# Kernel optimization log

Hardware: AMD Instinct MI355X
Metric: run time of the kernel (lower is better)

Reference implementation:

```python
import jax, jax.numpy as jnp
import numpy as np

EPS = 1e-8


def setup_inputs() -> dict:
    key = jax.random.key(0)
    ks = jax.random.split(key, 4)
    B, Cin, Cout, K, S, H, W = 16, 256, 256, 3, 512, 128, 128
    return {
        "x": jax.random.normal(ks[0], (B, Cin, H, W), dtype=jnp.float32),
        "style": jax.random.normal(ks[1], (B, S), dtype=jnp.float32),
        "weight": jax.random.normal(ks[2], (1, Cout, Cin, K, K), dtype=jnp.float32),
        "mod_w": jax.random.normal(ks[3], (Cin, S), dtype=jnp.float32) * (1.0 / np.sqrt(S)),
        "mod_b": jnp.zeros((Cin,), dtype=jnp.float32),
        "bias": jnp.zeros((1, Cout, 1, 1), dtype=jnp.float32),
    }


def reference(x, style, weight, mod_w, mod_b, bias):
    B, Cin, H, W = x.shape
    _, Cout, _, K, _ = weight.shape
    scale = 1.0 / np.sqrt(Cin * K * K)

    # modulation: Linear(style_dim -> in_channel)
    s = style @ mod_w.T + mod_b                      # [B, Cin]
    w = scale * weight * s[:, None, :, None, None]   # [B, Cout, Cin, K, K]
    demod = jax.lax.rsqrt(jnp.sum(w * w, axis=(2, 3, 4)) + EPS)  # [B, Cout]
    w = w * demod[:, :, None, None, None]

    # grouped conv with groups = batch (per-sample weights)
    w = w.reshape(B * Cout, Cin, K, K)
    xg = x.reshape(1, B * Cin, H, W)
    out = jax.lax.conv_general_dilated(
        xg, w,
        window_strides=(1, 1),
        padding=[(1, 1), (1, 1)],
        dimension_numbers=("NCHW", "OIHW", "NCHW"),
        feature_group_count=B,
    )
    Ho, Wo = out.shape[2], out.shape[3]
    out = out.reshape(B, Cout, Ho, Wo)
    return out + bias
```

## Files before the change

### kernel.cpp

```cpp
#include <hip/hip_runtime.h>
#include <stdint.h>

typedef unsigned short u16;
typedef __attribute__((ext_vector_type(8))) short short8;
typedef __attribute__((ext_vector_type(4))) float f32x4;

#define AS1 __attribute__((address_space(1)))
#define AS3 __attribute__((address_space(3)))

static __device__ __forceinline__ void gload_lds16(const void* g, void* l) {
  __builtin_amdgcn_global_load_lds((const AS1 void*)g, (AS3 void*)l, 16, 0, 0);
}

static __device__ __forceinline__ u16 bf16r(float f) {
  union { float f; uint32_t u; } c; c.f = f;
  uint32_t u = c.u;
  u += 0x7fffu + ((u >> 16) & 1u);
  return (u16)(u >> 16);
}

static constexpr int NB = 16, CIN = 256, COUT = 256, HW = 128, SDIM = 512;
static constexpr float SCALE = 1.0f / 48.0f;

__global__ void k_style(const float* __restrict__ style, const float* __restrict__ mod_w,
                        const float* __restrict__ mod_b, float* __restrict__ s) {
  int b = blockIdx.x, ci = threadIdx.x;
  const float4* st = (const float4*)(style + (size_t)b * SDIM);
  const float4* mw = (const float4*)(mod_w + (size_t)ci * SDIM);
  float acc = 0.f;
  #pragma unroll 4
  for (int j = 0; j < SDIM / 4; ++j) {
    float4 a = st[j], w = mw[j];
    acc += a.x * w.x + a.y * w.y + a.z * w.z + a.w * w.w;
  }
  s[b * CIN + ci] = acc + mod_b[ci];
}

__global__ void k_wmod(const float* __restrict__ weight, const float* __restrict__ s,
                       u16* __restrict__ Wb) {
  __shared__ float wld[CIN * 9];
  __shared__ float red[8];
  int bid = blockIdx.x;
  int b = bid >> 8, co = bid & 255;
  int t = threadIdx.x;
  const float* wsrc = weight + (size_t)co * (CIN * 9);
  for (int i = t; i < CIN * 9; i += 256) wld[i] = wsrc[i];
  __syncthreads();
  int ci = t;
  float sv = s[b * CIN + ci];
  float v[9];
  float sq = 0.f;
  #pragma unroll
  for (int k = 0; k < 9; ++k) {
    float w = SCALE * wld[ci * 9 + k] * sv;
    v[k] = w;
    sq += w * w;
  }
  #pragma unroll
  for (int off = 32; off; off >>= 1) sq += __shfl_down(sq, off);
  int lane = t & 63, wid = t >> 6;
  if (lane == 0) red[wid] = sq;
  __syncthreads();
  if (t == 0) red[4] = rsqrtf(red[0] + red[1] + red[2] + red[3] + 1e-8f);
  __syncthreads();
  float demod = red[4];
  #pragma unroll
  for (int k = 0; k < 9; ++k) {
    Wb[(((size_t)b * 9 + k) * COUT + co) * CIN + ci] = bf16r(v[k] * demod);
  }
}

__global__ void k_xt(const float* __restrict__ x, u16* __restrict__ xTp) {
  __shared__ u16 T[128 * 65];
  int bid = blockIdx.x;
  int b = bid >> 7, h = bid & 127;
  int t = threadIdx.x;
  size_t rowbase = (size_t)bid * 130 * CIN;
  xTp[rowbase + t] = 0;
  xTp[rowbase + (size_t)129 * CIN + t] = 0;
  for (int ci0 = 0; ci0 < CIN; ci0 += 64) {
    __syncthreads();
    #pragma unroll
    for (int i = 0; i < 8; ++i) {
      int idx = t + i * 256;
      int ci = idx >> 5, px4 = idx & 31;
      float4 v = *(const float4*)(x + (((size_t)b * CIN + ci0 + ci) * HW + h) * HW + px4 * 4);
      T[(px4 * 4 + 0) * 65 + ci] = bf16r(v.x);
      T[(px4 * 4 + 1) * 65 + ci] = bf16r(v.y);
      T[(px4 * 4 + 2) * 65 + ci] = bf16r(v.z);
      T[(px4 * 4 + 3) * 65 + ci] = bf16r(v.w);
    }
    __syncthreads();
    int ci = t & 63, pxo = t >> 6;
    #pragma unroll
    for (int i = 0; i < 32; ++i) {
      int px = i * 4 + pxo;
      xTp[rowbase + (size_t)(px + 1) * CIN + ci0 + ci] = T[px * 65 + ci];
    }
  }
}

__global__ __launch_bounds__(256, 2) void k_conv(const u16* __restrict__ Wb,
                                                 const u16* __restrict__ xTp,
                                                 const float* __restrict__ bias,
                                                 float* __restrict__ out) {
  __shared__ __align__(16) u16 As[128 * 64];
  __shared__ __align__(16) u16 Bs[128 * 64];
  int gid = blockIdx.x;
  int b = gid >> 8, r = gid & 255, cot = r >> 7, h = r & 127;
  int t = threadIdx.x, lane = t & 63, wid = t >> 6;
  int wr = wid >> 1, wc = wid & 1;

  f32x4 acc[4][4];
  #pragma unroll
  for (int i = 0; i < 4; ++i)
    #pragma unroll
    for (int j = 0; j < 4; ++j) acc[i][j] = (f32x4)0.f;

  int srow = wid * 8 + (lane >> 3);
  int scol = (lane & 7) * 8;

  for (int kh = 0; kh < 3; ++kh) {
    int hh = h + kh - 1;
    if ((unsigned)hh >= 128u) continue;
    for (int kw = 0; kw < 3; ++kw) {
      const u16* Ag0 = Wb + (((size_t)b * 9 + kh * 3 + kw) * COUT + cot * 128) * CIN;
      const u16* Bg0 = xTp + ((size_t)(b * 128 + hh) * 130 + kw) * CIN;
      for (int ci0 = 0; ci0 < CIN; ci0 += 64) {
        #pragma unroll
        for (int it = 0; it < 4; ++it) {
          int row = it * 32 + srow;
          gload_lds16(Ag0 + (size_t)row * CIN + ci0 + scol, &As[(it * 32 + wid * 8) * 64]);
        }
        #pragma unroll
        for (int it = 0; it < 4; ++it) {
          int row = it * 32 + srow;
          gload_lds16(Bg0 + (size_t)row * CIN + ci0 + scol, &Bs[(it * 32 + wid * 8) * 64]);
        }
        __syncthreads();
        #pragma unroll
        for (int kk = 0; kk < 2; ++kk) {
          short8 a[4], bb[4];
          #pragma unroll
          for (int mt = 0; mt < 4; ++mt)
            a[mt] = *(const short8*)&As[(wr * 64 + mt * 16 + (lane & 15)) * 64 + kk * 32 + (lane >> 4) * 8];
          #pragma unroll
          for (int nt = 0; nt < 4; ++nt)
            bb[nt] = *(const short8*)&Bs[(wc * 64 + nt * 16 + (lane & 15)) * 64 + kk * 32 + (lane >> 4) * 8];
          #pragma unroll
          for (int mt = 0; mt < 4; ++mt)
            #pragma unroll
            for (int nt = 0; nt < 4; ++nt)
              acc[mt][nt] = __builtin_amdgcn_mfma_f32_16x16x32_bf16(a[mt], bb[nt], acc[mt][nt], 0, 0, 0);
        }
        __syncthreads();
      }
    }
  }

  int colbase = wc * 64 + (lane & 15);
  int rowbase0 = cot * 128 + wr * 64 + ((lane >> 4) * 4);
  #pragma unroll
  for (int mt = 0; mt < 4; ++mt) {
    #pragma unroll
    for (int j = 0; j < 4; ++j) {
      int co = rowbase0 + mt * 16 + j;
      float bv = bias[co];
      float* orow = out + (((size_t)b * COUT + co) * HW + h) * HW;
      #pragma unroll
      for (int nt = 0; nt < 4; ++nt)
        orow[colbase + nt * 16] = acc[mt][nt][j] + bv;
    }
  }
}

extern "C" void kernel_launch(void* const* d_in, const int* in_sizes, int n_in,
                              void* d_out, int out_size, void* d_ws, size_t ws_size,
                              hipStream_t stream) {
  const float* x      = (const float*)d_in[0];
  const float* style  = (const float*)d_in[1];
  const float* weight = (const float*)d_in[2];
  const float* mod_w  = (const float*)d_in[3];
  const float* mod_b  = (const float*)d_in[4];
  const float* bias   = (const float*)d_in[5];
  float* out = (float*)d_out;

  char* ws = (char*)d_ws;
  float* s   = (float*)ws;
  u16* Wb    = (u16*)(ws + 16384);
  u16* xTp   = (u16*)(ws + 16384 + (size_t)NB * 9 * COUT * CIN * 2);

  k_style<<<NB, 256, 0, stream>>>(style, mod_w, mod_b, s);
  k_wmod<<<NB * COUT, 256, 0, stream>>>(weight, s, Wb);
  k_xt<<<NB * HW, 256, 0, stream>>>(x, xTp);
  k_conv<<<NB * 2 * HW, 256, 0, stream>>>(Wb, xTp, bias, out);
}
```

Measured before the change: 469.0 us.

## Restructure conv GEMM into 512-thread 256x128 tile with triple-buffered LDS pipeline

The conv kernel now uses 512-thread blocks that cover all 256 output channels for one image row, so each input tile is loaded once instead of twice. Global-to-LDS copies are triple-buffered with prefetch two k-steps ahead and explicit vmcnt waits, and MFMA phases run at raised wave priority. LDS columns are XOR-swizzled to avoid bank conflicts, and block IDs are remapped for locality. In exchange it needs 144KB of dynamic LDS at one block per CU, and it relies on hand-placed barriers and waitcnt values being correct.

```diff
diff --git a/kernel.cpp b/kernel.cpp
--- a/kernel.cpp
+++ b/kernel.cpp
@@ -100,16 +100,30 @@
   }
 }
 
-__global__ __launch_bounds__(256, 2) void k_conv(const u16* __restrict__ Wb,
+static constexpr int SLOTU = 24576;
+
+__global__ __launch_bounds__(512, 1) void k_conv(const u16* __restrict__ Wb,
                                                  const u16* __restrict__ xTp,
                                                  const float* __restrict__ bias,
                                                  float* __restrict__ out) {
-  __shared__ __align__(16) u16 As[128 * 64];
-  __shared__ __align__(16) u16 Bs[128 * 64];
-  int gid = blockIdx.x;
-  int b = gid >> 8, r = gid & 255, cot = r >> 7, h = r & 127;
+  extern __shared__ u16 lds[];
+  int bid = blockIdx.x;
+  int swz = (bid & 7) * 256 + (bid >> 3);
+  int b = swz >> 7, h = swz & 127;
+
   int t = threadIdx.x, lane = t & 63, wid = t >> 6;
   int wr = wid >> 1, wc = wid & 1;
+  int rowoff = wid * 8 + (lane >> 3);
+  int swzc = ((lane & 7) ^ (lane >> 3)) << 3;
+  int arow64 = (wr * 64 + (lane & 15)) * 64;
+  int brow64 = (wc * 64 + (lane & 15)) * 64;
+  int klo = (lane >> 4) * 8;
+  int cxor = (lane & 7) << 3;
+
+  const size_t wbB = (size_t)b * 9 * 256 * 256;
+
+  int ktbase = (h == 0) ? 12 : 0;
+  int nkt = 36 - ((h == 0) ? 12 : 0) - ((h == 127) ? 12 : 0);
 
   f32x4 acc[4][4];
   #pragma unroll
@@ -117,59 +131,114 @@
     #pragma unroll
     for (int j = 0; j < 4; ++j) acc[i][j] = (f32x4)0.f;
 
-  int srow = wid * 8 + (lane >> 3);
-  int scol = (lane & 7) * 8;
-
-  for (int kh = 0; kh < 3; ++kh) {
-    int hh = h + kh - 1;
-    if ((unsigned)hh >= 128u) continue;
-    for (int kw = 0; kw < 3; ++kw) {
-      const u16* Ag0 = Wb + (((size_t)b * 9 + kh * 3 + kw) * COUT + cot * 128) * CIN;
-      const u16* Bg0 = xTp + ((size_t)(b * 128 + hh) * 130 + kw) * CIN;
-      for (int ci0 = 0; ci0 < CIN; ci0 += 64) {
-        #pragma unroll
-        for (int it = 0; it < 4; ++it) {
-          int row = it * 32 + srow;
-          gload_lds16(Ag0 + (size_t)row * CIN + ci0 + scol, &As[(it * 32 + wid * 8) * 64]);
-        }
-        #pragma unroll
-        for (int it = 0; it < 4; ++it) {
-          int row = it * 32 + srow;
-          gload_lds16(Bg0 + (size_t)row * CIN + ci0 + scol, &Bs[(it * 32 + wid * 8) * 64]);
-        }
-        __syncthreads();
-        #pragma unroll
-        for (int kk = 0; kk < 2; ++kk) {
-          short8 a[4], bb[4];
-          #pragma unroll
-          for (int mt = 0; mt < 4; ++mt)
-            a[mt] = *(const short8*)&As[(wr * 64 + mt * 16 + (lane & 15)) * 64 + kk * 32 + (lane >> 4) * 8];
-          #pragma unroll
-          for (int nt = 0; nt < 4; ++nt)
-            bb[nt] = *(const short8*)&Bs[(wc * 64 + nt * 16 + (lane & 15)) * 64 + kk * 32 + (lane >> 4) * 8];
-          #pragma unroll
-          for (int mt = 0; mt < 4; ++mt)
-            #pragma unroll
-            for (int nt = 0; nt < 4; ++nt)
-              acc[mt][nt] = __builtin_amdgcn_mfma_f32_16x16x32_bf16(a[mt], bb[nt], acc[mt][nt], 0, 0, 0);
-        }
-        __syncthreads();
+  auto stage_ptrs = [&](int kta, const u16*& Asrc, const u16*& Bsrc) {
+    int kpos = kta >> 2, ci0 = (kta & 3) << 6;
+    int kh = kpos < 3 ? 0 : (kpos < 6 ? 1 : 2);
+    int kw = kpos - kh * 3;
+    Asrc = Wb + wbB + ((size_t)kpos * 256 + rowoff) * 256 + ci0 + swzc;
+    Bsrc = xTp + (((size_t)(b * 128 + h + kh - 1)) * 130 + kw + rowoff) * 256 + ci0 + swzc;
+  };
+
+  #pragma unroll
+  for (int p = 0; p < 2; ++p) {
+    const u16 *Asrc, *Bsrc;
+    stage_ptrs(ktbase + p, Asrc, Bsrc);
+    u16* A2 = lds + p * SLOTU;
+    u16* B2 = A2 + 16384;
+    #pragma unroll
+    for (int i = 0; i < 4; ++i)
+      gload_lds16(Asrc + (size_t)i * 16384, A2 + (i * 64 + wid * 8) * 64);
+    #pragma unroll
+    for (int i = 0; i < 2; ++i)
+      gload_lds16(Bsrc + (size_t)i * 16384, B2 + (i * 64 + wid * 8) * 64);
+  }
+  asm volatile("s_waitcnt vmcnt(6)" ::: "memory");
+  __builtin_amdgcn_s_barrier();
+  asm volatile("" ::: "memory");
+
+  int cur = 0;
+  for (int kt = 0; kt < nkt; ++kt) {
+    u16* A = lds + cur * SLOTU;
+    u16* Bl = A + 16384;
+    int s2 = (cur >= 1) ? cur - 1 : 2;
+    u16* A2 = lds + s2 * SLOTU;
+    u16* B2 = A2 + 16384;
+    bool pf = (kt + 2) < nkt;
+    const u16 *Asrc = nullptr, *Bsrc = nullptr;
+    if (pf) stage_ptrs(ktbase + kt + 2, Asrc, Bsrc);
+
+    short8 a[4][2], bb[2][2];
+    #pragma unroll
+    for (int mt = 0; mt < 4; ++mt)
+      #pragma unroll
+      for (int kk = 0; kk < 2; ++kk)
+        a[mt][kk] = *(const short8*)&A[arow64 + mt * 1024 + ((kk * 32 + klo) ^ cxor)];
+    #pragma unroll
+    for (int nt = 0; nt < 2; ++nt)
+      #pragma unroll
+      for (int kk = 0; kk < 2; ++kk)
+        bb[nt][kk] = *(const short8*)&Bl[brow64 + nt * 1024 + ((kk * 32 + klo) ^ cxor)];
+    if (pf) {
+      gload_lds16(Asrc + (size_t)0 * 16384, A2 + (0 * 64 + wid * 8) * 64);
+      gload_lds16(Asrc + (size_t)1 * 16384, A2 + (1 * 64 + wid * 8) * 64);
+      gload_lds16(Asrc + (size_t)2 * 16384, A2 + (2 * 64 + wid * 8) * 64);
+    }
+    asm volatile("" ::: "memory");
+    __builtin_amdgcn_s_barrier();
+    asm volatile("" ::: "memory");
+    __builtin_amdgcn_s_setprio(1);
+    #pragma unroll
+    for (int mt = 0; mt < 4; ++mt)
+      #pragma unroll
+      for (int nt = 0; nt < 2; ++nt) {
+        acc[mt][nt] = __builtin_amdgcn_mfma_f32_16x16x32_bf16(a[mt][0], bb[nt][0], acc[mt][nt], 0, 0, 0);
+        acc[mt][nt] = __builtin_amdgcn_mfma_f32_16x16x32_bf16(a[mt][1], bb[nt][1], acc[mt][nt], 0, 0, 0);
       }
-    }
-  }
-
-  int colbase = wc * 64 + (lane & 15);
-  int rowbase0 = cot * 128 + wr * 64 + ((lane >> 4) * 4);
+    __builtin_amdgcn_s_setprio(0);
+    asm volatile("" ::: "memory");
+    __builtin_amdgcn_s_barrier();
+    asm volatile("" ::: "memory");
+    #pragma unroll
+    for (int nt = 0; nt < 2; ++nt)
+      #pragma unroll
+      for (int kk = 0; kk < 2; ++kk)
+        bb[nt][kk] = *(const short8*)&Bl[brow64 + (2 + nt) * 1024 + ((kk * 32 + klo) ^ cxor)];
+    if (pf) {
+      gload_lds16(Asrc + (size_t)3 * 16384, A2 + (3 * 64 + wid * 8) * 64);
+      gload_lds16(Bsrc + (size_t)0 * 16384, B2 + (0 * 64 + wid * 8) * 64);
+      gload_lds16(Bsrc + (size_t)1 * 16384, B2 + (1 * 64 + wid * 8) * 64);
+    }
+    asm volatile("" ::: "memory");
+    __builtin_amdgcn_s_barrier();
+    asm volatile("" ::: "memory");
+    __builtin_amdgcn_s_setprio(1);
+    #pragma unroll
+    for (int mt = 0; mt < 4; ++mt)
+      #pragma unroll
+      for (int nt = 0; nt < 2; ++nt) {
+        acc[mt][2 + nt] = __builtin_amdgcn_mfma_f32_16x16x32_bf16(a[mt][0], bb[nt][0], acc[mt][2 + nt], 0, 0, 0);
+        acc[mt][2 + nt] = __builtin_amdgcn_mfma_f32_16x16x32_bf16(a[mt][1], bb[nt][1], acc[mt][2 + nt], 0, 0, 0);
+      }
+    __builtin_amdgcn_s_setprio(0);
+    asm volatile("" ::: "memory");
+    __builtin_amdgcn_s_barrier();
+    if (kt < nkt - 2) asm volatile("s_waitcnt vmcnt(6)" ::: "memory");
+    else              asm volatile("s_waitcnt vmcnt(0)" ::: "memory");
+    __builtin_amdgcn_s_barrier();
+    asm volatile("" ::: "memory");
+    cur = (cur < 2) ? cur + 1 : 0;
+  }
+
   #pragma unroll
   for (int mt = 0; mt < 4; ++mt) {
     #pragma unroll
     for (int j = 0; j < 4; ++j) {
-      int co = rowbase0 + mt * 16 + j;
+      int co = wr * 64 + mt * 16 + ((lane >> 4) * 4) + j;
       float bv = bias[co];
       float* orow = out + (((size_t)b * COUT + co) * HW + h) * HW;
       #pragma unroll
       for (int nt = 0; nt < 4; ++nt)
-        orow[colbase + nt * 16] = acc[mt][nt][j] + bv;
+        orow[wc * 64 + nt * 16 + (lane & 15)] = acc[mt][nt][j] + bv;
     }
   }
 }
@@ -190,8 +259,11 @@
   u16* Wb    = (u16*)(ws + 16384);
   u16* xTp   = (u16*)(ws + 16384 + (size_t)NB * 9 * COUT * CIN * 2);
 
+  (void)hipFuncSetAttribute((const void*)k_conv,
+                            hipFuncAttributeMaxDynamicSharedMemorySize, 3 * SLOTU * 2);
+
   k_style<<<NB, 256, 0, stream>>>(style, mod_w, mod_b, s);
   k_wmod<<<NB * COUT, 256, 0, stream>>>(weight, s, Wb);
   k_xt<<<NB * HW, 256, 0, stream>>>(x, xTp);
-  k_conv<<<NB * 2 * HW, 256, 0, stream>>>(Wb, xTp, bias, out);
-}
+  k_conv<<<NB * HW, 512, 3 * SLOTU * 2, stream>>>(Wb, xTp, bias, out);
+}
```

Result: no change. 464.8 us (-0.9%).

## Rewrite conv GEMM with 256x256 tiles, double-buffered LDS, swizzle and 2D padding

Applied to the files above, without the earlier changes.

The implicit-GEMM conv now computes all 256 output channels over two image rows (256 pixels) per 512-thread block, instead of 128 channels by one row. It double-buffers LDS so the next K-slice loads while MFMAs run, XOR-swizzles LDS columns to avoid bank conflicts, interleaves phases with barriers and setprio, and swizzles block order. The transposed input is now padded in both H and W so the kernel needs no boundary checks, at the cost of extra zero writes and 128KB of dynamic LDS per block. The larger tile raises data reuse and accumulator register pressure.

```diff
diff --git a/kernel.cpp b/kernel.cpp
--- a/kernel.cpp
+++ b/kernel.cpp
@@ -75,9 +75,17 @@
   int bid = blockIdx.x;
   int b = bid >> 7, h = bid & 127;
   int t = threadIdx.x;
-  size_t rowbase = (size_t)bid * 130 * CIN;
+  size_t rowbase = ((size_t)b * 130 + (h + 1)) * 130 * CIN;
   xTp[rowbase + t] = 0;
   xTp[rowbase + (size_t)129 * CIN + t] = 0;
+  if (h == 0) {
+    uint32_t* g = (uint32_t*)(xTp + (size_t)b * 130 * 130 * CIN);
+    for (int i = t; i < 130 * CIN / 2; i += 256) g[i] = 0;
+  }
+  if (h == 127) {
+    uint32_t* g = (uint32_t*)(xTp + ((size_t)b * 130 + 129) * 130 * CIN);
+    for (int i = t; i < 130 * CIN / 2; i += 256) g[i] = 0;
+  }
   for (int ci0 = 0; ci0 < CIN; ci0 += 64) {
     __syncthreads();
     #pragma unroll
@@ -100,76 +108,144 @@
   }
 }
 
-__global__ __launch_bounds__(256, 2) void k_conv(const u16* __restrict__ Wb,
+static constexpr int SLOTU = 32768;
+
+__global__ __launch_bounds__(512, 2) void k_conv(const u16* __restrict__ Wb,
                                                  const u16* __restrict__ xTp,
                                                  const float* __restrict__ bias,
                                                  float* __restrict__ out) {
-  __shared__ __align__(16) u16 As[128 * 64];
-  __shared__ __align__(16) u16 Bs[128 * 64];
-  int gid = blockIdx.x;
-  int b = gid >> 8, r = gid & 255, cot = r >> 7, h = r & 127;
+  extern __shared__ u16 lds[];
+  int bid = blockIdx.x;
+  int swz = (bid & 7) * 128 + (bid >> 3);
+  int b = swz >> 6, hp = swz & 63;
+  int h0 = hp * 2;
+
   int t = threadIdx.x, lane = t & 63, wid = t >> 6;
-  int wr = wid >> 1, wc = wid & 1;
-
-  f32x4 acc[4][4];
-  #pragma unroll
-  for (int i = 0; i < 4; ++i)
+  int wr = wid >> 2, wc = wid & 3;
+  int rowoff = wid * 8 + (lane >> 3);
+  int swzc = ((lane & 7) ^ (lane >> 3)) << 3;
+  int cxor = (lane & 7) << 3;
+  int klo = (lane >> 4) << 3;
+  int arow = (wr * 128 + (lane & 15)) * 64;
+  int brow = (wc * 64 + (lane & 15)) * 64;
+  const size_t wbB = (size_t)b * 9 * 65536;
+  const size_t xB = (size_t)b * 130 * 130 * 256;
+
+  f32x4 acc[8][4];
+  #pragma unroll
+  for (int i = 0; i < 8; ++i)
     #pragma unroll
     for (int j = 0; j < 4; ++j) acc[i][j] = (f32x4)0.f;
 
-  int srow = wid * 8 + (lane >> 3);
-  int scol = (lane & 7) * 8;
-
-  for (int kh = 0; kh < 3; ++kh) {
-    int hh = h + kh - 1;
-    if ((unsigned)hh >= 128u) continue;
-    for (int kw = 0; kw < 3; ++kw) {
-      const u16* Ag0 = Wb + (((size_t)b * 9 + kh * 3 + kw) * COUT + cot * 128) * CIN;
-      const u16* Bg0 = xTp + ((size_t)(b * 128 + hh) * 130 + kw) * CIN;
-      for (int ci0 = 0; ci0 < CIN; ci0 += 64) {
-        #pragma unroll
-        for (int it = 0; it < 4; ++it) {
-          int row = it * 32 + srow;
-          gload_lds16(Ag0 + (size_t)row * CIN + ci0 + scol, &As[(it * 32 + wid * 8) * 64]);
-        }
-        #pragma unroll
-        for (int it = 0; it < 4; ++it) {
-          int row = it * 32 + srow;
-          gload_lds16(Bg0 + (size_t)row * CIN + ci0 + scol, &Bs[(it * 32 + wid * 8) * 64]);
-        }
-        __syncthreads();
-        #pragma unroll
-        for (int kk = 0; kk < 2; ++kk) {
-          short8 a[4], bb[4];
-          #pragma unroll
-          for (int mt = 0; mt < 4; ++mt)
-            a[mt] = *(const short8*)&As[(wr * 64 + mt * 16 + (lane & 15)) * 64 + kk * 32 + (lane >> 4) * 8];
-          #pragma unroll
-          for (int nt = 0; nt < 4; ++nt)
-            bb[nt] = *(const short8*)&Bs[(wc * 64 + nt * 16 + (lane & 15)) * 64 + kk * 32 + (lane >> 4) * 8];
-          #pragma unroll
-          for (int mt = 0; mt < 4; ++mt)
-            #pragma unroll
-            for (int nt = 0; nt < 4; ++nt)
-              acc[mt][nt] = __builtin_amdgcn_mfma_f32_16x16x32_bf16(a[mt], bb[nt], acc[mt][nt], 0, 0, 0);
-        }
-        __syncthreads();
+  auto srcA = [&](int kta, int i) -> const u16* {
+    int kpos = kta >> 2, ci0 = (kta & 3) << 6;
+    return Wb + wbB + (size_t)kpos * 65536 + (size_t)(i * 64 + rowoff) * 256 + ci0 + swzc;
+  };
+  auto srcB = [&](int kta, int i) -> const u16* {
+    int kpos = kta >> 2, ci0 = (kta & 3) << 6;
+    int kh = kpos < 3 ? 0 : (kpos < 6 ? 1 : 2);
+    int kw = kpos - kh * 3;
+    int hh = h0 + kh + (i >> 1);
+    int pxp = kw + (i & 1) * 64 + rowoff;
+    return xTp + xB + ((size_t)hh * 130 + pxp) * 256 + ci0 + swzc;
+  };
+
+  {
+    u16* A2 = lds;
+    u16* B2 = lds + 16384;
+    #pragma unroll
+    for (int i = 0; i < 4; ++i) gload_lds16(srcA(0, i), A2 + (i * 64 + wid * 8) * 64);
+    #pragma unroll
+    for (int i = 0; i < 4; ++i) gload_lds16(srcB(0, i), B2 + (i * 64 + wid * 8) * 64);
+  }
+  asm volatile("s_waitcnt vmcnt(0)" ::: "memory");
+  __builtin_amdgcn_s_barrier();
+  asm volatile("" ::: "memory");
+
+  for (int kt = 0; kt < 36; ++kt) {
+    u16* Ac = lds + (kt & 1) * SLOTU;
+    u16* Bc = Ac + 16384;
+    u16* An = lds + ((kt & 1) ^ 1) * SLOTU;
+    u16* Bn = An + 16384;
+    bool pf = kt < 35;
+    int kta = kt + 1;
+
+    short8 bf[4][2], af0[2], af1[2];
+
+#define LD_A(M, KK) (*(const short8*)&Ac[arow + (M) * 1024 + (((KK) * 32 + klo) ^ cxor)])
+#define LD_B(N, KK) (*(const short8*)&Bc[brow + (N) * 1024 + (((KK) * 32 + klo) ^ cxor)])
+#define MFMA_PAIR(M)                                                                       \
+    _Pragma("unroll")                                                                      \
+    for (int nt = 0; nt < 4; ++nt) {                                                       \
+      acc[(M)][nt]     = __builtin_amdgcn_mfma_f32_16x16x32_bf16(af0[0], bf[nt][0], acc[(M)][nt], 0, 0, 0);     \
+      acc[(M)][nt]     = __builtin_amdgcn_mfma_f32_16x16x32_bf16(af0[1], bf[nt][1], acc[(M)][nt], 0, 0, 0);     \
+      acc[(M) + 1][nt] = __builtin_amdgcn_mfma_f32_16x16x32_bf16(af1[0], bf[nt][0], acc[(M) + 1][nt], 0, 0, 0); \
+      acc[(M) + 1][nt] = __builtin_amdgcn_mfma_f32_16x16x32_bf16(af1[1], bf[nt][1], acc[(M) + 1][nt], 0, 0, 0); \
+    }
+#define PHASE_BAR()                        \
+    asm volatile("" ::: "memory");         \
+    __builtin_amdgcn_s_barrier();          \
+    asm volatile("" ::: "memory");
+
+    #pragma unroll
+    for (int nt = 0; nt < 4; ++nt) { bf[nt][0] = LD_B(nt, 0); bf[nt][1] = LD_B(nt, 1); }
+    af0[0] = LD_A(0, 0); af0[1] = LD_A(0, 1);
+    af1[0] = LD_A(1, 0); af1[1] = LD_A(1, 1);
+    if (pf) {
+      #pragma unroll
+      for (int i = 0; i < 4; ++i) gload_lds16(srcA(kta, i), An + (i * 64 + wid * 8) * 64);
+    }
+    PHASE_BAR();
+    __builtin_amdgcn_s_setprio(1);
+    MFMA_PAIR(0);
+    __builtin_amdgcn_s_setprio(0);
+    PHASE_BAR();
+    af0[0] = LD_A(2, 0); af0[1] = LD_A(2, 1);
+    af1[0] = LD_A(3, 0); af1[1] = LD_A(3, 1);
+    if (pf) {
+      #pragma unroll
+      for (int i = 0; i < 4; ++i) gload_lds16(srcB(kta, i), Bn + (i * 64 + wid * 8) * 64);
+    }
+    PHASE_BAR();
+    __builtin_amdgcn_s_setprio(1);
+    MFMA_PAIR(2);
+    __builtin_amdgcn_s_setprio(0);
+    PHASE_BAR();
+    af0[0] = LD_A(4, 0); af0[1] = LD_A(4, 1);
+    af1[0] = LD_A(5, 0); af1[1] = LD_A(5, 1);
+    PHASE_BAR();
+    __builtin_amdgcn_s_setprio(1);
+    MFMA_PAIR(4);
+    __builtin_amdgcn_s_setprio(0);
+    PHASE_BAR();
+    af0[0] = LD_A(6, 0); af0[1] = LD_A(6, 1);
+    af1[0] = LD_A(7, 0); af1[1] = LD_A(7, 1);
+    PHASE_BAR();
+    __builtin_amdgcn_s_setprio(1);
+    MFMA_PAIR(6);
+    __builtin_amdgcn_s_setprio(0);
+    PHASE_BAR();
+    if (pf) asm volatile("s_waitcnt vmcnt(0)" ::: "memory");
+    __builtin_amdgcn_s_barrier();
+    asm volatile("" ::: "memory");
+#undef LD_A
+#undef LD_B
+#undef MFMA_PAIR
+#undef PHASE_BAR
+  }
+
+  #pragma unroll
+  for (int mt = 0; mt < 8; ++mt) {
+    #pragma unroll
+    for (int j = 0; j < 4; ++j) {
+      int co = wr * 128 + mt * 16 + ((lane >> 4) * 4) + j;
+      float bv = bias[co];
+      #pragma unroll
+      for (int nt = 0; nt < 4; ++nt) {
+        int px = wc * 64 + nt * 16 + (lane & 15);
+        int h = h0 + (px >> 7), w = px & 127;
+        out[(((size_t)b * COUT + co) * HW + h) * HW + w] = acc[mt][nt][j] + bv;
       }
-    }
-  }
-
-  int colbase = wc * 64 + (lane & 15);
-  int rowbase0 = cot * 128 + wr * 64 + ((lane >> 4) * 4);
-  #pragma unroll
-  for (int mt = 0; mt < 4; ++mt) {
-    #pragma unroll
-    for (int j = 0; j < 4; ++j) {
-      int co = rowbase0 + mt * 16 + j;
-      float bv = bias[co];
-      float* orow = out + (((size_t)b * COUT + co) * HW + h) * HW;
-      #pragma unroll
-      for (int nt = 0; nt < 4; ++nt)
-        orow[colbase + nt * 16] = acc[mt][nt][j] + bv;
     }
   }
 }
@@ -190,8 +266,11 @@
   u16* Wb    = (u16*)(ws + 16384);
   u16* xTp   = (u16*)(ws + 16384 + (size_t)NB * 9 * COUT * CIN * 2);
 
+  (void)hipFuncSetAttribute((const void*)k_conv,
+                            hipFuncAttributeMaxDynamicSharedMemorySize, 2 * SLOTU * 2);
+
   k_style<<<NB, 256, 0, stream>>>(style, mod_w, mod_b, s);
   k_wmod<<<NB * COUT, 256, 0, stream>>>(weight, s, Wb);
   k_xt<<<NB * HW, 256, 0, stream>>>(x, xTp);
-  k_conv<<<NB * 2 * HW, 256, 0, stream>>>(Wb, xTp, bias, out);
-}
+  k_conv<<<NB * (HW / 2), 512, 2 * SLOTU * 2, stream>>>(Wb, xTp, bias, out);
+}
```

New measurement: 411.8 us. 1.14x faster.

## Rewrite conv as LDS-free register double-buffered GEMM with full-height padded input

Applied to the files above, without the earlier changes.

The conv kernel drops LDS staging and barriers. Each wave now loads its MFMA operands straight from global memory into registers, double-buffered across K steps. Blocks grow to 512 threads and cover all 256 output channels by two image rows, with a swizzled block order for L2 locality. The transposed input buffer gains top and bottom zero-padding rows so the kh boundary branch goes away, at the cost of extra padding writes and larger per-thread register use (256 accumulator floats), which forces occupancy down to one block.

```diff
diff --git a/kernel.cpp b/kernel.cpp
--- a/kernel.cpp
+++ b/kernel.cpp
@@ -4,13 +4,6 @@
 typedef unsigned short u16;
 typedef __attribute__((ext_vector_type(8))) short short8;
 typedef __attribute__((ext_vector_type(4))) float f32x4;
-
-#define AS1 __attribute__((address_space(1)))
-#define AS3 __attribute__((address_space(3)))
-
-static __device__ __forceinline__ void gload_lds16(const void* g, void* l) {
-  __builtin_amdgcn_global_load_lds((const AS1 void*)g, (AS3 void*)l, 16, 0, 0);
-}
 
 static __device__ __forceinline__ u16 bf16r(float f) {
   union { float f; uint32_t u; } c; c.f = f;
@@ -75,9 +68,17 @@
   int bid = blockIdx.x;
   int b = bid >> 7, h = bid & 127;
   int t = threadIdx.x;
-  size_t rowbase = (size_t)bid * 130 * CIN;
+  size_t rowbase = ((size_t)b * 130 + (h + 1)) * 130 * CIN;
   xTp[rowbase + t] = 0;
   xTp[rowbase + (size_t)129 * CIN + t] = 0;
+  if (h == 0) {
+    uint32_t* g = (uint32_t*)(xTp + (size_t)b * 130 * 130 * CIN);
+    for (int i = t; i < 130 * CIN / 2; i += 256) g[i] = 0;
+  }
+  if (h == 127) {
+    uint32_t* g = (uint32_t*)(xTp + ((size_t)b * 130 + 129) * 130 * CIN);
+    for (int i = t; i < 130 * CIN / 2; i += 256) g[i] = 0;
+  }
   for (int ci0 = 0; ci0 < CIN; ci0 += 64) {
     __syncthreads();
     #pragma unroll
@@ -100,76 +101,90 @@
   }
 }
 
-__global__ __launch_bounds__(256, 2) void k_conv(const u16* __restrict__ Wb,
+__global__ __launch_bounds__(512, 1) void k_conv(const u16* __restrict__ Wb,
                                                  const u16* __restrict__ xTp,
                                                  const float* __restrict__ bias,
                                                  float* __restrict__ out) {
-  __shared__ __align__(16) u16 As[128 * 64];
-  __shared__ __align__(16) u16 Bs[128 * 64];
-  int gid = blockIdx.x;
-  int b = gid >> 8, r = gid & 255, cot = r >> 7, h = r & 127;
+  int bid = blockIdx.x;
+  int swz = (bid & 7) * 128 + (bid >> 3);
+  int b = swz >> 6, hp = swz & 63;
+  int h0 = hp * 2;
+
   int t = threadIdx.x, lane = t & 63, wid = t >> 6;
-  int wr = wid >> 1, wc = wid & 1;
-
-  f32x4 acc[4][4];
-  #pragma unroll
-  for (int i = 0; i < 4; ++i)
+  int wr = wid >> 2, wc = wid & 3;
+  int l15 = lane & 15, seg = lane >> 4;
+
+  const u16* Ab = Wb + (size_t)b * 9 * 65536;
+  const u16* Bb = xTp + (size_t)b * 130 * 130 * 256;
+
+  int aoff = (wr * 128 + l15) * 256 + seg * 8;
+  int boff = ((wc & 1) * 64 + l15) * 256 + seg * 8;
+  int hrow = h0 + (wc >> 1);
+
+  f32x4 acc[8][4];
+  #pragma unroll
+  for (int i = 0; i < 8; ++i)
     #pragma unroll
     for (int j = 0; j < 4; ++j) acc[i][j] = (f32x4)0.f;
 
-  int srow = wid * 8 + (lane >> 3);
-  int scol = (lane & 7) * 8;
-
-  for (int kh = 0; kh < 3; ++kh) {
-    int hh = h + kh - 1;
-    if ((unsigned)hh >= 128u) continue;
-    for (int kw = 0; kw < 3; ++kw) {
-      const u16* Ag0 = Wb + (((size_t)b * 9 + kh * 3 + kw) * COUT + cot * 128) * CIN;
-      const u16* Bg0 = xTp + ((size_t)(b * 128 + hh) * 130 + kw) * CIN;
-      for (int ci0 = 0; ci0 < CIN; ci0 += 64) {
-        #pragma unroll
-        for (int it = 0; it < 4; ++it) {
-          int row = it * 32 + srow;
-          gload_lds16(Ag0 + (size_t)row * CIN + ci0 + scol, &As[(it * 32 + wid * 8) * 64]);
-        }
-        #pragma unroll
-        for (int it = 0; it < 4; ++it) {
-          int row = it * 32 + srow;
-          gload_lds16(Bg0 + (size_t)row * CIN + ci0 + scol, &Bs[(it * 32 + wid * 8) * 64]);
-        }
-        __syncthreads();
-        #pragma unroll
-        for (int kk = 0; kk < 2; ++kk) {
-          short8 a[4], bb[4];
-          #pragma unroll
-          for (int mt = 0; mt < 4; ++mt)
-            a[mt] = *(const short8*)&As[(wr * 64 + mt * 16 + (lane & 15)) * 64 + kk * 32 + (lane >> 4) * 8];
-          #pragma unroll
-          for (int nt = 0; nt < 4; ++nt)
-            bb[nt] = *(const short8*)&Bs[(wc * 64 + nt * 16 + (lane & 15)) * 64 + kk * 32 + (lane >> 4) * 8];
-          #pragma unroll
-          for (int mt = 0; mt < 4; ++mt)
-            #pragma unroll
-            for (int nt = 0; nt < 4; ++nt)
-              acc[mt][nt] = __builtin_amdgcn_mfma_f32_16x16x32_bf16(a[mt], bb[nt], acc[mt][nt], 0, 0, 0);
-        }
-        __syncthreads();
+  short8 cA[8], cB[4], nA[8], nB[4];
+
+#define LOADA(DST, HT)                                                          \
+  do {                                                                          \
+    int kt_ = (HT) >> 1, kk_ = (HT) & 1;                                        \
+    int kpos_ = kt_ >> 2, ci0_ = (kt_ & 3) << 6;                                \
+    const u16* p_ = Ab + kpos_ * 65536 + ci0_ + kk_ * 32 + aoff;                \
+    _Pragma("unroll")                                                           \
+    for (int mt = 0; mt < 8; ++mt) DST[mt] = *(const short8*)(p_ + mt * 4096);  \
+  } while (0)
+#define LOADB(DST, HT)                                                          \
+  do {                                                                          \
+    int kt_ = (HT) >> 1, kk_ = (HT) & 1;                                        \
+    int kpos_ = kt_ >> 2, ci0_ = (kt_ & 3) << 6;                                \
+    int kh_ = kpos_ < 3 ? 0 : (kpos_ < 6 ? 1 : 2);                              \
+    int kw_ = kpos_ - kh_ * 3;                                                  \
+    const u16* p_ = Bb + ((size_t)(hrow + kh_) * 130 + kw_) * 256               \
+                       + ci0_ + kk_ * 32 + boff;                                \
+    _Pragma("unroll")                                                           \
+    for (int nt = 0; nt < 4; ++nt) DST[nt] = *(const short8*)(p_ + nt * 4096);  \
+  } while (0)
+#define MF(SA, SB)                                                              \
+  _Pragma("unroll")                                                             \
+  for (int mt = 0; mt < 8; ++mt)                                                \
+    _Pragma("unroll")                                                           \
+    for (int nt = 0; nt < 4; ++nt)                                              \
+      acc[mt][nt] =                                                             \
+          __builtin_amdgcn_mfma_f32_16x16x32_bf16(SA[mt], SB[nt], acc[mt][nt], 0, 0, 0);
+
+  LOADA(cA, 0);
+  LOADB(cB, 0);
+  #pragma unroll 1
+  for (int ht = 0; ht < 72; ht += 2) {
+    LOADA(nA, ht + 1);
+    LOADB(nB, ht + 1);
+    MF(cA, cB);
+    if (ht + 2 < 72) {
+      LOADA(cA, ht + 2);
+      LOADB(cB, ht + 2);
+    }
+    MF(nA, nB);
+  }
+#undef LOADA
+#undef LOADB
+#undef MF
+
+  #pragma unroll
+  for (int mt = 0; mt < 8; ++mt) {
+    #pragma unroll
+    for (int j = 0; j < 4; ++j) {
+      int co = wr * 128 + mt * 16 + ((lane >> 4) * 4) + j;
+      float bv = bias[co];
+      #pragma unroll
+      for (int nt = 0; nt < 4; ++nt) {
+        int px = wc * 64 + nt * 16 + l15;
+        int h = h0 + (px >> 7), w = px & 127;
+        out[(((size_t)b * COUT + co) * HW + h) * HW + w] = acc[mt][nt][j] + bv;
       }
-    }
-  }
-
-  int colbase = wc * 64 + (lane & 15);
-  int rowbase0 = cot * 128 + wr * 64 + ((lane >> 4) * 4);
-  #pragma unroll
-  for (int mt = 0; mt < 4; ++mt) {
-    #pragma unroll
-    for (int j = 0; j < 4; ++j) {
-      int co = rowbase0 + mt * 16 + j;
-      float bv = bias[co];
-      float* orow = out + (((size_t)b * COUT + co) * HW + h) * HW;
-      #pragma unroll
-      for (int nt = 0; nt < 4; ++nt)
-        orow[colbase + nt * 16] = acc[mt][nt][j] + bv;
     }
   }
 }
@@ -193,5 +208,5 @@
   k_style<<<NB, 256, 0, stream>>>(style, mod_w, mod_b, s);
   k_wmod<<<NB * COUT, 256, 0, stream>>>(weight, s, Wb);
   k_xt<<<NB * HW, 256, 0, stream>>>(x, xTp);
-  k_conv<<<NB * 2 * HW, 256, 0, stream>>>(Wb, xTp, bias, out);
-}
+  k_conv<<<NB * (HW / 2), 512, 0, stream>>>(Wb, xTp, bias, out);
+}
```

Result: slower. 918.5 us (+95.8%).
